# Kernel optimization log

Measured on AMD Instinct MI355X. Metric: run time of the kernel, lower is better.

The kernel has to match this reference:

```python
import jax, jax.numpy as jnp
import numpy as np

LAMBDA_COORD = 5.0
LAMBDA_NOOBJ = 0.5
EPS = 1e-16


def setup_inputs() -> dict:
    key = jax.random.key(0)
    k1, k2, k3 = jax.random.split(key, 3)
    B, H, W, C, T = 64, 80, 80, 80, 50
    predictions = jax.random.normal(k1, (B, H * W, 5 + C), dtype=jnp.float32)
    cls_id = jax.random.randint(k2, (B, T), 0, C).astype(jnp.float32)
    # cx, cy, w, h normalized to (0,1); margin keeps every target in-grid
    boxes = jax.random.uniform(k3, (B, T, 4), minval=0.05, maxval=0.95, dtype=jnp.float32)
    targets = jnp.concatenate([cls_id[..., None], boxes], axis=-1)  # [B, T, 5]
    return {"predictions": predictions, "targets": targets, "H": H, "W": W}


def reference(predictions, targets, H, W):
    B, HW, D = predictions.shape
    T = targets.shape[1]
    num_classes = D - 5

    cls_id = targets[..., 0].astype(jnp.int32)           # [B, T]
    cx, cy = targets[..., 1], targets[..., 2]
    w, h = targets[..., 3], targets[..., 4]

    # grid assignment (all targets in-bounds by construction)
    gx = jnp.floor(cx * W).astype(jnp.int32)
    gy = jnp.floor(cy * H).astype(jnp.int32)
    gi = gy * W + gx                                     # [B, T] flat cell index

    tx = cx * W - gx
    ty = cy * H - gy
    tw = jnp.log(w * W + EPS)
    th = jnp.log(h * H + EPS)

    # gather predictions at assigned cells -> [B, T, D]
    g = jnp.take_along_axis(predictions, gi[:, :, None], axis=1)
    pred_xy = jax.nn.sigmoid(g[..., :2])
    pred_wh = g[..., 2:4]
    pred_cls = g[..., 5:]

    # per-target MSE (mean over the 2 coords, as F.mse_loss), summed over targets
    xy_loss = jnp.sum(jnp.mean((pred_xy - jnp.stack([tx, ty], axis=-1)) ** 2, axis=-1))
    wh_loss = jnp.sum(jnp.mean((pred_wh - jnp.stack([tw, th], axis=-1)) ** 2, axis=-1))

    # per-target cross entropy, summed
    logp = jax.nn.log_softmax(pred_cls, axis=-1)
    cls_loss = -jnp.sum(jnp.take_along_axis(logp, cls_id[..., None], axis=-1))

    # objectness masks via scatter
    obj_mask = jnp.zeros((B, HW), dtype=bool).at[jnp.arange(B)[:, None], gi].set(True)
    noobj_mask = ~obj_mask

    conf_logit = predictions[..., 4]                     # [B, HW]
    # BCE(sigmoid(x), 1) = softplus(-x); BCE(sigmoid(x), 0) = softplus(x)
    n_obj_cells = jnp.sum(obj_mask)
    n_noobj = jnp.sum(noobj_mask)
    conf_obj = jnp.sum(jax.nn.softplus(-conf_logit) * obj_mask) / jnp.maximum(n_obj_cells, 1)
    conf_noobj = jnp.sum(jax.nn.softplus(conf_logit) * noobj_mask) / jnp.maximum(n_noobj, 1)

    num_obj = max(B * T, 1)  # all targets valid
    total = (LAMBDA_COORD * (xy_loss + wh_loss) / num_obj
             + conf_obj / num_obj
             + LAMBDA_NOOBJ * conf_noobj / jnp.maximum(n_noobj, 1)
             + cls_loss / num_obj)
    return total
```

## Files before the change

kernel.cpp:

```cpp
#include <hip/hip_runtime.h>
#include <math.h>

#define NB    64
#define NH    80
#define NW    80
#define NHW   6400
#define NT    50
#define ND    85
#define NCELL (NB * NHW)
#define NTGT  (NB * NT)
#define GRID  400

__device__ __forceinline__ float softplus_f(float x) {
    return fmaxf(x, 0.0f) + log1pf(expf(-fabsf(x)));
}

__global__ __launch_bounds__(1024)
void main_kernel(const float* __restrict__ pred,
                 const float* __restrict__ tgt,
                 float* __restrict__ partials) {
    const int bid  = blockIdx.x;
    const int tid  = threadIdx.x;
    const int lane = tid & 63;
    const int wib  = tid >> 6;

    __shared__ float s_red[6];
    if (tid < 6) s_red[tid] = 0.0f;
    __syncthreads();

    if (wib < 8) {
        const int i = bid * 8 + wib;
        const int b = i / NT;
        const int t = i - b * NT;

        const float* tp = tgt + (size_t)i * 5;
        float cx = tp[1];
        float cy = tp[2];
        int gx = (int)floorf(cx * (float)NW);
        int gy = (int)floorf(cy * (float)NH);
        int gi = gy * NW + gx;

        bool match = false;
        if (lane < t) {
            const float* tj = tgt + ((size_t)b * NT + lane) * 5;
            int gxj = (int)floorf(tj[1] * (float)NW);
            int gyj = (int)floorf(tj[2] * (float)NH);
            match = (gyj * NW + gxj) == gi;
        }
        unsigned long long mb = __ballot(match);

        const float* g = pred + ((size_t)b * NHW + gi) * ND;
        float e0 = g[lane];
        float e1 = (lane < ND - 64) ? g[64 + lane] : 0.0f;

        float s = ((lane >= 5)      ? expf(e0) : 0.0f)
                + ((lane < ND - 64) ? expf(e1) : 0.0f);
        #pragma unroll
        for (int off = 32; off; off >>= 1) s += __shfl_xor(s, off, 64);

        if (lane == 0) {
            int   cid  = (int)tp[0];
            float w    = tp[3];
            float h    = tp[4];
            float gsel = g[5 + cid];
            float g0 = g[0], g1 = g[1], g2 = g[2], g3 = g[3], confp = g[4];

            float cls_v = -(gsel - logf(s));

            float px = 1.0f / (1.0f + expf(-g0));
            float py = 1.0f / (1.0f + expf(-g1));
            float tx = cx * (float)NW - (float)gx;
            float ty = cy * (float)NH - (float)gy;
            float tw = logf(w * (float)NW + 1e-16f);
            float th = logf(h * (float)NH + 1e-16f);
            float xy = 0.5f * ((px - tx) * (px - tx) + (py - ty) * (py - ty));
            float wh = 0.5f * ((g2 - tw) * (g2 - tw) + (g3 - th) * (g3 - th));

            atomicAdd(&s_red[0], xy + wh);
            atomicAdd(&s_red[1], cls_v);
            if (mb == 0ull) {
                atomicAdd(&s_red[2], softplus_f(-confp));
                atomicAdd(&s_red[3], 1.0f);
                atomicAdd(&s_red[4], softplus_f(confp));
            }
        }
    }

    {
        const int c = bid * 1024 + tid;
        float sp = softplus_f(pred[(size_t)c * ND + 4]);
        #pragma unroll
        for (int off = 32; off; off >>= 1) sp += __shfl_xor(sp, off, 64);
        if (lane == 0) atomicAdd(&s_red[5], sp);
    }

    __syncthreads();
    if (tid < 6) partials[(size_t)tid * GRID + bid] = s_red[tid];
}

__global__ __launch_bounds__(512)
void final_kernel(const float* __restrict__ partials,
                  float* __restrict__ out) {
    const int tid  = threadIdx.x;
    const int lane = tid & 63;
    const int wib  = tid >> 6;

    float a[6];
    #pragma unroll
    for (int k = 0; k < 6; ++k)
        a[k] = (tid < GRID) ? partials[(size_t)k * GRID + tid] : 0.0f;
    #pragma unroll
    for (int k = 0; k < 6; ++k) {
        #pragma unroll
        for (int off = 32; off; off >>= 1) a[k] += __shfl_xor(a[k], off, 64);
    }

    __shared__ float sh[8][6];
    if (lane == 0) {
        #pragma unroll
        for (int k = 0; k < 6; ++k) sh[wib][k] = a[k];
    }
    __syncthreads();

    if (tid == 0) {
        float t0 = 0, t1 = 0, t2 = 0, t3 = 0, t4 = 0, t5 = 0;
        #pragma unroll
        for (int wv = 0; wv < 8; ++wv) {
            t0 += sh[wv][0]; t1 += sh[wv][1]; t2 += sh[wv][2];
            t3 += sh[wv][3]; t4 += sh[wv][4]; t5 += sh[wv][5];
        }
        float coord = t0, cls = t1, objs = t2, nobj = t3, corr = t4, allsp = t5;

        float noobj = allsp - corr;
        float nno   = (float)NCELL - nobj;

        float conf_obj   = objs  / fmaxf(nobj, 1.0f);
        float conf_noobj = noobj / fmaxf(nno,  1.0f);
        const float num_obj = (float)(NB * NT);

        out[0] = 5.0f * coord / num_obj
               + conf_obj / num_obj
               + 0.5f * conf_noobj / fmaxf(nno, 1.0f)
               + cls / num_obj;
    }
}

extern "C" void kernel_launch(void* const* d_in, const int* in_sizes, int n_in,
                              void* d_out, int out_size, void* d_ws, size_t ws_size,
                              hipStream_t stream) {
    const float* pred = (const float*)d_in[0];
    const float* tgt  = (const float*)d_in[1];
    float* partials   = (float*)d_ws;

    main_kernel <<<GRID, 1024, 0, stream>>>(pred, tgt, partials);
    final_kernel<<<1,     512, 0, stream>>>(partials, (float*)d_out);
}
```

Baseline: 17.87 us.

## Fuse final reduction into main kernel via atomic last-block completion

Removes the second reduction kernel. Each block first recomputes the global count of unique object cells from all targets in shared memory, so it can normalise its own partial sum. It then atomically adds that term to a global accumulator, and the last block to finish writes the output and resets the counters. This saves one kernel launch and the partials round trip. In exchange, every block redundantly scans all 3200 targets for duplicates (a serial loop of up to 50 compares per target), and the result depends on float atomic ordering.

```diff
diff --git a/kernel.cpp b/kernel.cpp
--- a/kernel.cpp
+++ b/kernel.cpp
@@ -11,27 +11,63 @@
 #define NTGT  (NB * NT)
 #define GRID  400
 
+__device__ float g_total = 0.0f;
+__device__ int   g_cnt   = 0;
+
 __device__ __forceinline__ float softplus_f(float x) {
     return fmaxf(x, 0.0f) + log1pf(expf(-fabsf(x)));
 }
 
 __global__ __launch_bounds__(1024)
-void main_kernel(const float* __restrict__ pred,
-                 const float* __restrict__ tgt,
-                 float* __restrict__ partials) {
+void fused_kernel(const float* __restrict__ pred,
+                  const float* __restrict__ tgt,
+                  float* __restrict__ out) {
     const int bid  = blockIdx.x;
     const int tid  = threadIdx.x;
     const int lane = tid & 63;
     const int wib  = tid >> 6;
 
-    __shared__ float s_red[6];
+    __shared__ int           s_gi[NTGT];
+    __shared__ unsigned char s_u[NTGT];
+    __shared__ float         s_red[6];
+    __shared__ int           s_wu[16];
+    __shared__ int           s_nobj;
+
     if (tid < 6) s_red[tid] = 0.0f;
+
+    for (int r = tid; r < NTGT; r += 1024) {
+        const float* tr = tgt + (size_t)r * 5;
+        int gx = (int)floorf(tr[1] * (float)NW);
+        int gy = (int)floorf(tr[2] * (float)NH);
+        s_gi[r] = gy * NW + gx;
+    }
     __syncthreads();
+
+    int my_u = 0;
+    for (int r = tid; r < NTGT; r += 1024) {
+        int p    = r % NT;
+        int base = r - p;
+        int gi   = s_gi[r];
+        bool uniq = true;
+        for (int j = 0; j < p; ++j)
+            if (s_gi[base + j] == gi) { uniq = false; break; }
+        s_u[r] = (unsigned char)uniq;
+        my_u += uniq ? 1 : 0;
+    }
+    #pragma unroll
+    for (int off = 32; off; off >>= 1) my_u += __shfl_xor(my_u, off, 64);
+    if (lane == 0) s_wu[wib] = my_u;
+    __syncthreads();
+    if (tid == 0) {
+        int n = 0;
+        #pragma unroll
+        for (int wv = 0; wv < 16; ++wv) n += s_wu[wv];
+        s_nobj = n;
+    }
 
     if (wib < 8) {
         const int i = bid * 8 + wib;
         const int b = i / NT;
-        const int t = i - b * NT;
 
         const float* tp = tgt + (size_t)i * 5;
         float cx = tp[1];
@@ -39,15 +75,6 @@
         int gx = (int)floorf(cx * (float)NW);
         int gy = (int)floorf(cy * (float)NH);
         int gi = gy * NW + gx;
-
-        bool match = false;
-        if (lane < t) {
-            const float* tj = tgt + ((size_t)b * NT + lane) * 5;
-            int gxj = (int)floorf(tj[1] * (float)NW);
-            int gyj = (int)floorf(tj[2] * (float)NH);
-            match = (gyj * NW + gxj) == gi;
-        }
-        unsigned long long mb = __ballot(match);
 
         const float* g = pred + ((size_t)b * NHW + gi) * ND;
         float e0 = g[lane];
@@ -78,9 +105,8 @@
 
             atomicAdd(&s_red[0], xy + wh);
             atomicAdd(&s_red[1], cls_v);
-            if (mb == 0ull) {
+            if (s_u[i]) {
                 atomicAdd(&s_red[2], softplus_f(-confp));
-                atomicAdd(&s_red[3], 1.0f);
                 atomicAdd(&s_red[4], softplus_f(confp));
             }
         }
@@ -95,53 +121,31 @@
     }
 
     __syncthreads();
-    if (tid < 6) partials[(size_t)tid * GRID + bid] = s_red[tid];
-}
-
-__global__ __launch_bounds__(512)
-void final_kernel(const float* __restrict__ partials,
-                  float* __restrict__ out) {
-    const int tid  = threadIdx.x;
-    const int lane = tid & 63;
-    const int wib  = tid >> 6;
-
-    float a[6];
-    #pragma unroll
-    for (int k = 0; k < 6; ++k)
-        a[k] = (tid < GRID) ? partials[(size_t)k * GRID + tid] : 0.0f;
-    #pragma unroll
-    for (int k = 0; k < 6; ++k) {
-        #pragma unroll
-        for (int off = 32; off; off >>= 1) a[k] += __shfl_xor(a[k], off, 64);
-    }
-
-    __shared__ float sh[8][6];
-    if (lane == 0) {
-        #pragma unroll
-        for (int k = 0; k < 6; ++k) sh[wib][k] = a[k];
-    }
-    __syncthreads();
 
     if (tid == 0) {
-        float t0 = 0, t1 = 0, t2 = 0, t3 = 0, t4 = 0, t5 = 0;
-        #pragma unroll
-        for (int wv = 0; wv < 8; ++wv) {
-            t0 += sh[wv][0]; t1 += sh[wv][1]; t2 += sh[wv][2];
-            t3 += sh[wv][3]; t4 += sh[wv][4]; t5 += sh[wv][5];
+        float coord = s_red[0];
+        float cls   = s_red[1];
+        float objs  = s_red[2];
+        float corr  = s_red[4];
+        float allsp = s_red[5];
+
+        float n_obj = (float)s_nobj;
+        float nno   = (float)NCELL - n_obj;
+
+        float term = 5.0f * coord / 3200.0f
+                   + (objs / fmaxf(n_obj, 1.0f)) / 3200.0f
+                   + 0.5f * ((allsp - corr) / fmaxf(nno, 1.0f)) / fmaxf(nno, 1.0f)
+                   + cls / 3200.0f;
+
+        atomicAdd(&g_total, term);
+        asm volatile("s_waitcnt vmcnt(0)" ::: "memory");
+        int old = atomicAdd(&g_cnt, 1);
+        if (old == GRID - 1) {
+            float tot = atomicAdd(&g_total, 0.0f);
+            out[0] = tot;
+            atomicExch(&g_total, 0.0f);
+            atomicExch(&g_cnt, 0);
         }
-        float coord = t0, cls = t1, objs = t2, nobj = t3, corr = t4, allsp = t5;
-
-        float noobj = allsp - corr;
-        float nno   = (float)NCELL - nobj;
-
-        float conf_obj   = objs  / fmaxf(nobj, 1.0f);
-        float conf_noobj = noobj / fmaxf(nno,  1.0f);
-        const float num_obj = (float)(NB * NT);
-
-        out[0] = 5.0f * coord / num_obj
-               + conf_obj / num_obj
-               + 0.5f * conf_noobj / fmaxf(nno, 1.0f)
-               + cls / num_obj;
     }
 }
 
@@ -150,8 +154,5 @@
                               hipStream_t stream) {
     const float* pred = (const float*)d_in[0];
     const float* tgt  = (const float*)d_in[1];
-    float* partials   = (float*)d_ws;
-
-    main_kernel <<<GRID, 1024, 0, stream>>>(pred, tgt, partials);
-    final_kernel<<<1,     512, 0, stream>>>(partials, (float*)d_out);
+    fused_kernel<<<GRID, 1024, 0, stream>>>(pred, tgt, (float*)d_out);
 }
```

Measured after the change: 38.11 us. 113% more time.
